# Optimization experiments

Measured on AMD Instinct MI355X. Metric: run time of the kernel, lower is better.

The kernel has to match this reference:

```python
import jax, jax.numpy as jnp
import numpy as np

N_NODES = 50000
N_EDGES = 300000
D_IN = 256
D_HID = 256
N_LAYERS = 3
D_OUT = 32
NUM_GRAPHS = 512


def setup_inputs() -> dict:
    key = jax.random.key(0)
    ks = jax.random.split(key, 10)
    x = jax.random.normal(ks[0], (N_NODES, D_IN), dtype=jnp.float32)
    edge_index = jax.random.randint(ks[1], (2, N_EDGES), 0, N_NODES, dtype=jnp.int64)
    batch = jnp.sort(jax.random.randint(ks[2], (N_NODES,), 0, NUM_GRAPHS, dtype=jnp.int64))
    # GraphConv params: out_i = relu(lin_rel(sum_j x_j) + lin_root(x_i)), bias in lin_rel.
    # in_channels == hidden_channels so all nc layers stack into one tensor.
    s = 1.0 / np.sqrt(D_HID)
    W_rel = jax.random.normal(ks[3], (N_LAYERS, D_HID, D_HID), dtype=jnp.float32) * s
    W_root = jax.random.normal(ks[4], (N_LAYERS, D_HID, D_HID), dtype=jnp.float32) * s
    b_conv = jax.random.normal(ks[5], (N_LAYERS, D_HID), dtype=jnp.float32) * s
    W1 = jax.random.normal(ks[6], (D_HID, 4 * D_HID), dtype=jnp.float32) * s
    b1 = jnp.zeros((4 * D_HID,), dtype=jnp.float32)
    W2 = jax.random.normal(ks[7], (4 * D_HID, D_OUT), dtype=jnp.float32) * (1.0 / np.sqrt(4 * D_HID))
    b2 = jnp.zeros((D_OUT,), dtype=jnp.float32)
    return {"x": x, "edge_index": edge_index, "batch": batch,
            "W_rel": W_rel, "W_root": W_root, "b_conv": b_conv,
            "W1": W1, "b1": b1, "W2": W2, "b2": b2,
            "num_graphs": NUM_GRAPHS}


def reference(x, edge_index, batch, W_rel, W_root, b_conv, W1, b1, W2, b2, num_graphs):
    src, dst = edge_index[0], edge_index[1]
    n = x.shape[0]
    # stacked GraphConv(aggr='add') layers with ReLU
    for i in range(W_rel.shape[0]):
        aggr = jax.ops.segment_sum(x[src], dst, num_segments=n)  # [N, d] gather+scatter-add
        x = jax.nn.relu(aggr @ W_rel[i] + x @ W_root[i] + b_conv[i])
    # global_add_pool over graph ids
    pooled = jax.ops.segment_sum(x, batch, num_segments=num_graphs)  # [G, d]
    h = jax.nn.relu(pooled @ W1 + b1)
    return jax.nn.sigmoid(h @ W2 + b2)
```

## Files before the change

### kernel.cpp

```cpp
#include <hip/hip_runtime.h>
#include <math.h>

#define NNODES 50000
#define MPAD   50048
#define D      256
#define K2     512
#define NEDGES 300000
#define NGRAPH 512
#define NLAYERS 3

#define SCB    256
#define NSCB   ((NNODES + SCB - 1) / SCB)

typedef __bf16 bf16x8 __attribute__((ext_vector_type(8)));
typedef float  f32x4  __attribute__((ext_vector_type(4)));

__device__ __forceinline__ ushort f2bf(float f) {
    unsigned u = __float_as_uint(f);
    unsigned r = (u + 0x7FFFu + ((u >> 16) & 1u)) >> 16;
    return (ushort)r;
}
__device__ __forceinline__ float bf2f(ushort b) {
    return __uint_as_float(((unsigned)b) << 16);
}

__device__ __forceinline__ void stage16(const ushort* g, ushort* l) {
    __builtin_amdgcn_global_load_lds(
        (const __attribute__((address_space(1))) unsigned*)g,
        (__attribute__((address_space(3))) unsigned*)l, 16, 0, 0);
}

__global__ __launch_bounds__(256)
void hist_kernel(const int* __restrict__ dst, int* __restrict__ deg, int nE) {
    int e = blockIdx.x * 256 + threadIdx.x;
    if (e < nE) atomicAdd(&deg[dst[e]], 1);
}

__global__ __launch_bounds__(SCB)
void scan_part_kernel(const int* __restrict__ deg, int* __restrict__ bsum) {
    __shared__ int red[SCB];
    int t = threadIdx.x;
    int i = blockIdx.x * SCB + t;
    red[t] = (i < NNODES) ? deg[i] : 0;
    __syncthreads();
#pragma unroll
    for (int off = SCB / 2; off > 0; off >>= 1) {
        if (t < off) red[t] += red[t + off];
        __syncthreads();
    }
    if (t == 0) bsum[blockIdx.x] = red[0];
}

__global__ __launch_bounds__(256)
void scan_bsum_kernel(const int* __restrict__ bsum, int* __restrict__ boff) {
    __shared__ int p[256];
    int t = threadIdx.x;
    p[t] = (t < NSCB) ? bsum[t] : 0;
    __syncthreads();
    for (int off = 1; off < 256; off <<= 1) {
        int v = (t >= off) ? p[t - off] : 0;
        __syncthreads();
        p[t] += v;
        __syncthreads();
    }
    if (t < NSCB) boff[t] = (t == 0) ? 0 : p[t - 1];
}

__global__ __launch_bounds__(SCB)
void scan_final_kernel(const int* __restrict__ deg, const int* __restrict__ boff,
                       int* __restrict__ row_start, int* __restrict__ cursor) {
    __shared__ int p[SCB];
    int t = threadIdx.x;
    int i = blockIdx.x * SCB + t;
    int v = (i < NNODES) ? deg[i] : 0;
    p[t] = v;
    __syncthreads();
    for (int off = 1; off < SCB; off <<= 1) {
        int u = (t >= off) ? p[t - off] : 0;
        __syncthreads();
        p[t] += u;
        __syncthreads();
    }
    int excl = boff[blockIdx.x] + p[t] - v;
    if (i < NNODES) {
        row_start[i] = excl;
        cursor[i] = excl;
    }
    if (blockIdx.x == 0 && t == 0) row_start[NNODES] = NEDGES;
}

__global__ __launch_bounds__(256)
void fill_kernel(const int* __restrict__ src, const int* __restrict__ dst,
                 int* __restrict__ cursor, int* __restrict__ e_src, int nE) {
    int e = blockIdx.x * 256 + threadIdx.x;
    if (e < nE) {
        int pos = atomicAdd(&cursor[dst[e]], 1);
        e_src[pos] = src[e];
    }
}

__global__ __launch_bounds__(256)
void gstart_kernel(const int* __restrict__ batch, int* __restrict__ gstart) {
    int g = blockIdx.x * 256 + threadIdx.x;
    if (g > NGRAPH) return;
    if (g == NGRAPH) { gstart[g] = NNODES; return; }
    int lo = 0, hi = NNODES;
    while (lo < hi) { int mid = (lo + hi) >> 1; if (batch[mid] < g) lo = mid + 1; else hi = mid; }
    gstart[g] = lo;
}

__global__ __launch_bounds__(256)
void prep_w_kernel(const float* __restrict__ W_rel, const float* __restrict__ W_root,
                   ushort* __restrict__ Wh, ushort* __restrict__ Wl) {
    int i = blockIdx.x * 256 + threadIdx.x;
    if (i >= NLAYERS * D * K2) return;
    int L = i / (D * K2);
    int rem = i % (D * K2);
    int n = rem / K2;
    int k = rem % K2;
    float v = (k < D) ? W_rel[(size_t)L * D * D + (size_t)k * D + n]
                      : W_root[(size_t)L * D * D + (size_t)(k - D) * D + n];
    ushort hi = f2bf(v);
    float  lo = v - bf2f(hi);
    Wh[i] = hi;
    Wl[i] = f2bf(lo);
}

__global__ __launch_bounds__(256)
void gather_f32_kernel(const float* __restrict__ x,
                       const int* __restrict__ row_start,
                       const int* __restrict__ e_src,
                       float* __restrict__ aggr) {
    int t = threadIdx.x;
    int n = blockIdx.x * 4 + (t >> 6);
    if (n >= NNODES) return;
    int lane = t & 63;
    int beg = row_start[n], end = row_start[n + 1];
    float a0 = 0.f, a1 = 0.f, a2 = 0.f, a3 = 0.f;
    int j = beg;
    for (; j + 4 <= end; j += 4) {
        int s0 = e_src[j], s1 = e_src[j + 1], s2 = e_src[j + 2], s3 = e_src[j + 3];
        float4 v0 = *reinterpret_cast<const float4*>(x + (size_t)s0 * D + lane * 4);
        float4 v1 = *reinterpret_cast<const float4*>(x + (size_t)s1 * D + lane * 4);
        float4 v2 = *reinterpret_cast<const float4*>(x + (size_t)s2 * D + lane * 4);
        float4 v3 = *reinterpret_cast<const float4*>(x + (size_t)s3 * D + lane * 4);
        a0 += v0.x + v1.x + v2.x + v3.x;
        a1 += v0.y + v1.y + v2.y + v3.y;
        a2 += v0.z + v1.z + v2.z + v3.z;
        a3 += v0.w + v1.w + v2.w + v3.w;
    }
    for (; j < end; ++j) {
        int s = e_src[j];
        float4 v = *reinterpret_cast<const float4*>(x + (size_t)s * D + lane * 4);
        a0 += v.x; a1 += v.y; a2 += v.z; a3 += v.w;
    }
    float4 o; o.x = a0; o.y = a1; o.z = a2; o.w = a3;
    *reinterpret_cast<float4*>(aggr + (size_t)n * D + lane * 4) = o;
}

#define GBM 64
#define GBN 128
#define GBK 32

__global__ __launch_bounds__(256)
void gemm_split_kernel(const float* __restrict__ A,
                       const float* __restrict__ X,
                       const ushort* __restrict__ Wh,
                       const ushort* __restrict__ Wl,
                       const float* __restrict__ bias,
                       float* __restrict__ out) {
    __shared__ ushort Ah[GBM * GBK];
    __shared__ ushort Al[GBM * GBK];
    __shared__ ushort Bh[GBN * GBK];
    __shared__ ushort Bl[GBN * GBK];

    int t = threadIdx.x;
    int wid = t >> 6, lane = t & 63;
    int m0 = blockIdx.x * GBM;
    int n0 = blockIdx.y * GBN;
    int wr = wid >> 1, wc = wid & 1;
    int r = lane & 15, kq = lane >> 4;

    f32x4 acc[2][4];
#pragma unroll
    for (int m = 0; m < 2; ++m)
#pragma unroll
        for (int n = 0; n < 4; ++n)
            acc[m][n] = (f32x4){0.f, 0.f, 0.f, 0.f};

    int arow = t >> 2;
    int acb  = t & 3;
    int ap   = ((arow >> 1) & 3) ^ acb;
    int gr   = m0 + arow;
    bool arow_ok = (gr < NNODES);

    for (int k0 = 0; k0 < K2; k0 += GBK) {
        const float* Asrc = (k0 < D) ? A : X;
        int kk = k0 & (D - 1);

#pragma unroll
        for (int op = 0; op < 2; ++op) {
            int idx = op * 256 + t;
            int row = idx >> 2, sub = idx & 3;
            int kh = ((row >> 1) & 3) ^ sub;
            stage16(Wh + (size_t)(n0 + row) * K2 + k0 + kh * 8, Bh + (size_t)idx * 8);
            stage16(Wl + (size_t)(n0 + row) * K2 + k0 + kh * 8, Bl + (size_t)idx * 8);
        }

        {
            const float* base = Asrc + (size_t)gr * D + kk + acb * 8;
            float4 v0, v1;
            if (arow_ok) {
                v0 = *reinterpret_cast<const float4*>(base + 0);
                v1 = *reinterpret_cast<const float4*>(base + 4);
            } else {
                v0 = v1 = make_float4(0.f, 0.f, 0.f, 0.f);
            }
            float vv[8] = {v0.x, v0.y, v0.z, v0.w, v1.x, v1.y, v1.z, v1.w};
            ushort hi[8], lo[8];
#pragma unroll
            for (int i = 0; i < 8; ++i) {
                hi[i] = f2bf(vv[i]);
                lo[i] = f2bf(vv[i] - bf2f(hi[i]));
            }
            *reinterpret_cast<uint4*>(&Ah[arow * GBK + ap * 8]) = *reinterpret_cast<const uint4*>(hi);
            *reinterpret_cast<uint4*>(&Al[arow * GBK + ap * 8]) = *reinterpret_cast<const uint4*>(lo);
        }
        __syncthreads();

        bf16x8 ah[2], al[2], bh[4], bl[4];
#pragma unroll
        for (int m = 0; m < 2; ++m) {
            int row = wr * 32 + m * 16 + r;
            int off = row * GBK + ((((row >> 1) & 3) ^ kq) * 8);
            ah[m] = *reinterpret_cast<const bf16x8*>(&Ah[off]);
            al[m] = *reinterpret_cast<const bf16x8*>(&Al[off]);
        }
#pragma unroll
        for (int n = 0; n < 4; ++n) {
            int row = wc * 64 + n * 16 + r;
            int off = row * GBK + ((((row >> 1) & 3) ^ kq) * 8);
            bh[n] = *reinterpret_cast<const bf16x8*>(&Bh[off]);
            bl[n] = *reinterpret_cast<const bf16x8*>(&Bl[off]);
        }
        __syncthreads();

#pragma unroll
        for (int m = 0; m < 2; ++m)
#pragma unroll
            for (int n = 0; n < 4; ++n) {
                acc[m][n] = __builtin_amdgcn_mfma_f32_16x16x32_bf16(ah[m], bh[n], acc[m][n], 0, 0, 0);
                acc[m][n] = __builtin_amdgcn_mfma_f32_16x16x32_bf16(ah[m], bl[n], acc[m][n], 0, 0, 0);
                acc[m][n] = __builtin_amdgcn_mfma_f32_16x16x32_bf16(al[m], bh[n], acc[m][n], 0, 0, 0);
            }
    }

#pragma unroll
    for (int n = 0; n < 4; ++n) {
        int col = n0 + wc * 64 + n * 16 + r;
        float bv = bias[col];
#pragma unroll
        for (int m = 0; m < 2; ++m) {
            int rbase = m0 + wr * 32 + m * 16 + kq * 4;
#pragma unroll
            for (int j = 0; j < 4; ++j) {
                int rr = rbase + j;
                if (rr < NNODES)
                    out[(size_t)rr * D + col] = fmaxf(acc[m][n][j] + bv, 0.f);
            }
        }
    }
}

__global__ __launch_bounds__(256)
void pool_mlp_kernel(const float* __restrict__ x, const int* __restrict__ gstart,
                     const float* __restrict__ W1, const float* __restrict__ b1,
                     const float* __restrict__ W2, const float* __restrict__ b2,
                     float* __restrict__ out) {
    __shared__ float red[4][D];
    __shared__ float p[D];
    __shared__ float h[4 * D];
    int g = blockIdx.x;
    int t = threadIdx.x, wid = t >> 6, lane = t & 63;

    int beg = gstart[g], end = gstart[g + 1];
    float a0 = 0.f, a1 = 0.f, a2 = 0.f, a3 = 0.f;
    for (int r = beg + wid; r < end; r += 4) {
        float4 v = *reinterpret_cast<const float4*>(x + (size_t)r * D + lane * 4);
        a0 += v.x; a1 += v.y; a2 += v.z; a3 += v.w;
    }
    red[wid][lane * 4 + 0] = a0;
    red[wid][lane * 4 + 1] = a1;
    red[wid][lane * 4 + 2] = a2;
    red[wid][lane * 4 + 3] = a3;
    __syncthreads();
    p[t] = red[0][t] + red[1][t] + red[2][t] + red[3][t];
    __syncthreads();

    float4 acc = make_float4(0.f, 0.f, 0.f, 0.f);
    for (int k = 0; k < D; ++k) {
        float4 w = *reinterpret_cast<const float4*>(W1 + (size_t)k * 1024 + t * 4);
        float pv = p[k];
        acc.x += pv * w.x; acc.y += pv * w.y; acc.z += pv * w.z; acc.w += pv * w.w;
    }
    float4 b = *reinterpret_cast<const float4*>(b1 + t * 4);
    h[t * 4 + 0] = fmaxf(acc.x + b.x, 0.f);
    h[t * 4 + 1] = fmaxf(acc.y + b.y, 0.f);
    h[t * 4 + 2] = fmaxf(acc.z + b.z, 0.f);
    h[t * 4 + 3] = fmaxf(acc.w + b.w, 0.f);
    __syncthreads();

    float* red2 = &red[0][0];
    int c = t & 31, kc = t >> 5;
    float s = 0.f;
    for (int k = kc * 128; k < kc * 128 + 128; ++k)
        s += h[k] * W2[(size_t)k * 32 + c];
    red2[kc * 32 + c] = s;
    __syncthreads();
    if (t < 32) {
        float v = b2[t];
#pragma unroll
        for (int i = 0; i < 8; ++i) v += red2[i * 32 + t];
        out[(size_t)g * 32 + t] = 1.f / (1.f + expf(-v));
    }
}

extern "C" void kernel_launch(void* const* d_in, const int* in_sizes, int n_in,
                              void* d_out, int out_size, void* d_ws, size_t ws_size,
                              hipStream_t stream) {
    const float* x      = (const float*)d_in[0];
    const int*   ei     = (const int*)d_in[1];
    const int*   batch  = (const int*)d_in[2];
    const float* W_rel  = (const float*)d_in[3];
    const float* W_root = (const float*)d_in[4];
    const float* b_conv = (const float*)d_in[5];
    const float* W1     = (const float*)d_in[6];
    const float* b1     = (const float*)d_in[7];
    const float* W2     = (const float*)d_in[8];
    const float* b2     = (const float*)d_in[9];
    float* outp = (float*)d_out;

    const size_t NF = (size_t)MPAD * D;
    float* aggr   = (float*)d_ws;
    float* buf0   = aggr + NF;
    float* buf1   = buf0 + NF;
    ushort* Wh    = (ushort*)(buf1 + NF);
    ushort* Wl    = Wh + (size_t)NLAYERS * D * K2;
    int* deg       = (int*)(Wl + (size_t)NLAYERS * D * K2);
    int* row_start = deg + NNODES;
    int* cursor    = row_start + NNODES + 1;
    int* e_src     = cursor + NNODES;
    int* gstart    = e_src + NEDGES;
    int* bsum      = gstart + NGRAPH + 1;
    int* boff      = bsum + NSCB;

    const int* srcp = ei;
    const int* dstp = ei + NEDGES;

    hipMemsetAsync(deg, 0, NNODES * sizeof(int), stream);
    hist_kernel<<<(NEDGES + 255) / 256, 256, 0, stream>>>(dstp, deg, NEDGES);
    scan_part_kernel<<<NSCB, SCB, 0, stream>>>(deg, bsum);
    scan_bsum_kernel<<<1, 256, 0, stream>>>(bsum, boff);
    scan_final_kernel<<<NSCB, SCB, 0, stream>>>(deg, boff, row_start, cursor);
    fill_kernel<<<(NEDGES + 255) / 256, 256, 0, stream>>>(srcp, dstp, cursor, e_src, NEDGES);
    gstart_kernel<<<3, 256, 0, stream>>>(batch, gstart);

    prep_w_kernel<<<(NLAYERS * D * K2 + 255) / 256, 256, 0, stream>>>(W_rel, W_root, Wh, Wl);

    int gatherBlocks = (NNODES + 3) / 4;
    dim3 ggrid(MPAD / GBM, D / GBN);

    const float* cur = x;
    float* nxt = buf0;
    for (int L = 0; L < NLAYERS; ++L) {
        gather_f32_kernel<<<gatherBlocks, 256, 0, stream>>>(cur, row_start, e_src, aggr);
        gemm_split_kernel<<<ggrid, 256, 0, stream>>>(aggr, cur,
                                                     Wh + (size_t)L * D * K2,
                                                     Wl + (size_t)L * D * K2,
                                                     b_conv + (size_t)L * D,
                                                     nxt);
        cur = nxt;
        nxt = (nxt == buf0) ? buf1 : buf0;
    }

    pool_mlp_kernel<<<NGRAPH, 256, 0, stream>>>(cur, gstart, W1, b1, W2, b2, outp);
}
```

Before: 431.2 us.

## Split pool+MLP into pooling, MFMA split-bf16 GEMM for W1, and small W2 kernel

The fused per-graph pool/MLP kernel is split into three kernels: segment pooling into a buffer, a tiled MFMA GEMM for the 512x256x1024 first MLP layer using hi/lo bf16 splitting, and a separate W2+sigmoid kernel. Before, every one of the 512 blocks streamed all of W1 (1MB) with scalar FMAs. The new GEMM reuses W1 tiles across graphs and runs on matrix cores. In exchange it adds two launches, a W1 prep kernel and intermediate buffers.

```diff
diff --git a/kernel.cpp b/kernel.cpp
--- a/kernel.cpp
+++ b/kernel.cpp
@@ -124,6 +124,19 @@
     float  lo = v - bf2f(hi);
     Wh[i] = hi;
     Wl[i] = f2bf(lo);
+}
+
+__global__ __launch_bounds__(256)
+void prep_w1_kernel(const float* __restrict__ W1,
+                    ushort* __restrict__ W1h, ushort* __restrict__ W1l) {
+    int i = blockIdx.x * 256 + threadIdx.x;
+    if (i >= 1024 * D) return;
+    int n = i >> 8;
+    int k = i & (D - 1);
+    float v = W1[(size_t)k * 1024 + n];
+    ushort hi = f2bf(v);
+    W1h[i] = hi;
+    W1l[i] = f2bf(v - bf2f(hi));
 }
 
 __global__ __launch_bounds__(256)
@@ -273,16 +286,11 @@
 }
 
 __global__ __launch_bounds__(256)
-void pool_mlp_kernel(const float* __restrict__ x, const int* __restrict__ gstart,
-                     const float* __restrict__ W1, const float* __restrict__ b1,
-                     const float* __restrict__ W2, const float* __restrict__ b2,
-                     float* __restrict__ out) {
+void pool_seg_kernel(const float* __restrict__ x, const int* __restrict__ gstart,
+                     float* __restrict__ pooled) {
     __shared__ float red[4][D];
-    __shared__ float p[D];
-    __shared__ float h[4 * D];
     int g = blockIdx.x;
     int t = threadIdx.x, wid = t >> 6, lane = t & 63;
-
     int beg = gstart[g], end = gstart[g + 1];
     float a0 = 0.f, a1 = 0.f, a2 = 0.f, a3 = 0.f;
     for (int r = beg + wid; r < end; r += 4) {
@@ -294,33 +302,125 @@
     red[wid][lane * 4 + 2] = a2;
     red[wid][lane * 4 + 3] = a3;
     __syncthreads();
-    p[t] = red[0][t] + red[1][t] + red[2][t] + red[3][t];
-    __syncthreads();
-
-    float4 acc = make_float4(0.f, 0.f, 0.f, 0.f);
-    for (int k = 0; k < D; ++k) {
-        float4 w = *reinterpret_cast<const float4*>(W1 + (size_t)k * 1024 + t * 4);
-        float pv = p[k];
-        acc.x += pv * w.x; acc.y += pv * w.y; acc.z += pv * w.z; acc.w += pv * w.w;
-    }
-    float4 b = *reinterpret_cast<const float4*>(b1 + t * 4);
-    h[t * 4 + 0] = fmaxf(acc.x + b.x, 0.f);
-    h[t * 4 + 1] = fmaxf(acc.y + b.y, 0.f);
-    h[t * 4 + 2] = fmaxf(acc.z + b.z, 0.f);
-    h[t * 4 + 3] = fmaxf(acc.w + b.w, 0.f);
-    __syncthreads();
-
-    float* red2 = &red[0][0];
+    float s = red[0][t] + red[1][t] + red[2][t] + red[3][t];
+    pooled[(size_t)g * D + t] = s;
+}
+
+__global__ __launch_bounds__(256)
+void mlp1_gemm_kernel(const float* __restrict__ P,
+                      const ushort* __restrict__ W1h,
+                      const ushort* __restrict__ W1l,
+                      const float* __restrict__ b1,
+                      float* __restrict__ h) {
+    __shared__ ushort Ah[GBM * GBK];
+    __shared__ ushort Al[GBM * GBK];
+    __shared__ ushort Bh[GBN * GBK];
+    __shared__ ushort Bl[GBN * GBK];
+
+    int t = threadIdx.x;
+    int wid = t >> 6, lane = t & 63;
+    int m0 = blockIdx.x * GBM;
+    int n0 = blockIdx.y * GBN;
+    int wr = wid >> 1, wc = wid & 1;
+    int r = lane & 15, kq = lane >> 4;
+
+    f32x4 acc[2][4];
+#pragma unroll
+    for (int m = 0; m < 2; ++m)
+#pragma unroll
+        for (int n = 0; n < 4; ++n)
+            acc[m][n] = (f32x4){0.f, 0.f, 0.f, 0.f};
+
+    int arow = t >> 2;
+    int acb  = t & 3;
+    int ap   = ((arow >> 1) & 3) ^ acb;
+    int gr   = m0 + arow;
+
+    for (int k0 = 0; k0 < D; k0 += GBK) {
+#pragma unroll
+        for (int op = 0; op < 2; ++op) {
+            int idx = op * 256 + t;
+            int row = idx >> 2, sub = idx & 3;
+            int kh = ((row >> 1) & 3) ^ sub;
+            stage16(W1h + (size_t)(n0 + row) * D + k0 + kh * 8, Bh + (size_t)idx * 8);
+            stage16(W1l + (size_t)(n0 + row) * D + k0 + kh * 8, Bl + (size_t)idx * 8);
+        }
+        {
+            const float* base = P + (size_t)gr * D + k0 + acb * 8;
+            float4 v0 = *reinterpret_cast<const float4*>(base + 0);
+            float4 v1 = *reinterpret_cast<const float4*>(base + 4);
+            float vv[8] = {v0.x, v0.y, v0.z, v0.w, v1.x, v1.y, v1.z, v1.w};
+            ushort hi[8], lo[8];
+#pragma unroll
+            for (int i = 0; i < 8; ++i) {
+                hi[i] = f2bf(vv[i]);
+                lo[i] = f2bf(vv[i] - bf2f(hi[i]));
+            }
+            *reinterpret_cast<uint4*>(&Ah[arow * GBK + ap * 8]) = *reinterpret_cast<const uint4*>(hi);
+            *reinterpret_cast<uint4*>(&Al[arow * GBK + ap * 8]) = *reinterpret_cast<const uint4*>(lo);
+        }
+        __syncthreads();
+
+        bf16x8 ah[2], al[2], bh[4], bl[4];
+#pragma unroll
+        for (int m = 0; m < 2; ++m) {
+            int row = wr * 32 + m * 16 + r;
+            int off = row * GBK + ((((row >> 1) & 3) ^ kq) * 8);
+            ah[m] = *reinterpret_cast<const bf16x8*>(&Ah[off]);
+            al[m] = *reinterpret_cast<const bf16x8*>(&Al[off]);
+        }
+#pragma unroll
+        for (int n = 0; n < 4; ++n) {
+            int row = wc * 64 + n * 16 + r;
+            int off = row * GBK + ((((row >> 1) & 3) ^ kq) * 8);
+            bh[n] = *reinterpret_cast<const bf16x8*>(&Bh[off]);
+            bl[n] = *reinterpret_cast<const bf16x8*>(&Bl[off]);
+        }
+        __syncthreads();
+
+#pragma unroll
+        for (int m = 0; m < 2; ++m)
+#pragma unroll
+            for (int n = 0; n < 4; ++n) {
+                acc[m][n] = __builtin_amdgcn_mfma_f32_16x16x32_bf16(ah[m], bh[n], acc[m][n], 0, 0, 0);
+                acc[m][n] = __builtin_amdgcn_mfma_f32_16x16x32_bf16(ah[m], bl[n], acc[m][n], 0, 0, 0);
+                acc[m][n] = __builtin_amdgcn_mfma_f32_16x16x32_bf16(al[m], bh[n], acc[m][n], 0, 0, 0);
+            }
+    }
+
+#pragma unroll
+    for (int n = 0; n < 4; ++n) {
+        int col = n0 + wc * 64 + n * 16 + r;
+        float bv = b1[col];
+#pragma unroll
+        for (int m = 0; m < 2; ++m) {
+            int rbase = m0 + wr * 32 + m * 16 + kq * 4;
+#pragma unroll
+            for (int j = 0; j < 4; ++j) {
+                int rr = rbase + j;
+                h[(size_t)rr * 1024 + col] = fmaxf(acc[m][n][j] + bv, 0.f);
+            }
+        }
+    }
+}
+
+__global__ __launch_bounds__(256)
+void mlp2_kernel(const float* __restrict__ h, const float* __restrict__ W2,
+                 const float* __restrict__ b2, float* __restrict__ out) {
+    __shared__ float red[8][32];
+    int g = blockIdx.x, t = threadIdx.x;
     int c = t & 31, kc = t >> 5;
     float s = 0.f;
+    const float* hr = h + (size_t)g * 1024;
+#pragma unroll 4
     for (int k = kc * 128; k < kc * 128 + 128; ++k)
-        s += h[k] * W2[(size_t)k * 32 + c];
-    red2[kc * 32 + c] = s;
+        s += hr[k] * W2[(size_t)k * 32 + c];
+    red[kc][c] = s;
     __syncthreads();
     if (t < 32) {
         float v = b2[t];
 #pragma unroll
-        for (int i = 0; i < 8; ++i) v += red2[i * 32 + t];
+        for (int i = 0; i < 8; ++i) v += red[i][t];
         out[(size_t)g * 32 + t] = 1.f / (1.f + expf(-v));
     }
 }
@@ -346,7 +446,11 @@
     float* buf1   = buf0 + NF;
     ushort* Wh    = (ushort*)(buf1 + NF);
     ushort* Wl    = Wh + (size_t)NLAYERS * D * K2;
-    int* deg       = (int*)(Wl + (size_t)NLAYERS * D * K2);
+    ushort* W1h   = Wl + (size_t)NLAYERS * D * K2;
+    ushort* W1l   = W1h + (size_t)1024 * D;
+    float* pooled = (float*)(W1l + (size_t)1024 * D);
+    float* hbuf   = pooled + (size_t)NGRAPH * D;
+    int* deg       = (int*)(hbuf + (size_t)NGRAPH * 1024);
     int* row_start = deg + NNODES;
     int* cursor    = row_start + NNODES + 1;
     int* e_src     = cursor + NNODES;
@@ -366,6 +470,7 @@
     gstart_kernel<<<3, 256, 0, stream>>>(batch, gstart);
 
     prep_w_kernel<<<(NLAYERS * D * K2 + 255) / 256, 256, 0, stream>>>(W_rel, W_root, Wh, Wl);
+    prep_w1_kernel<<<(1024 * D + 255) / 256, 256, 0, stream>>>(W1, W1h, W1l);
 
     int gatherBlocks = (NNODES + 3) / 4;
     dim3 ggrid(MPAD / GBM, D / GBN);
@@ -383,5 +488,7 @@
         nxt = (nxt == buf0) ? buf1 : buf0;
     }
 
-    pool_mlp_kernel<<<NGRAPH, 256, 0, stream>>>(cur, gstart, W1, b1, W2, b2, outp);
-}
+    pool_seg_kernel<<<NGRAPH, 256, 0, stream>>>(cur, gstart, pooled);
+    mlp1_gemm_kernel<<<dim3(NGRAPH / GBM, 1024 / GBN), 256, 0, stream>>>(pooled, W1h, W1l, b1, hbuf);
+    mlp2_kernel<<<NGRAPH, 256, 0, stream>>>(hbuf, W2, b2, outp);
+}
```

After: 409.9 us, median of 2. 5.0% less time.
